# Optimization experiments

Measured on AMD Instinct MI355X. Metric: run time of the kernel, lower is better.

The kernel has to match this reference:

```python
import jax, jax.numpy as jnp
import numpy as np

B, L, H, A = 2, 384, 256, 14  # batch, total residues (binder+target), hidden, atoms/residue


def setup_inputs() -> dict:
    key = jax.random.key(0)
    ks = jax.random.split(key, 8)
    s = 1.0 / np.sqrt(H)
    h = jax.random.normal(ks[0], (B, L, H), jnp.float32)          # encoder output
    X = jax.random.normal(ks[1], (B, L, A, 3), jnp.float32)       # coordinates
    mask = jnp.ones((B, L), jnp.int32)                             # residue validity mask
    Wx_w = jax.random.normal(ks[2], (H, H), jnp.float32) * s
    Wx_b = jnp.zeros((H,), jnp.float32)
    Ux_w = jax.random.normal(ks[3], (H, H), jnp.float32) * s
    Ux_b = jnp.zeros((H,), jnp.float32)
    Tx_w = jax.random.normal(ks[4], (A, H), jnp.float32) * s
    Tx_b = jnp.zeros((A,), jnp.float32)
    return dict(h=h, X=X, mask=mask, Wx_w=Wx_w, Wx_b=Wx_b,
                Ux_w=Ux_w, Ux_b=Ux_b, Tx_w=Tx_w, Tx_b=Tx_b)


def reference(h, X, mask, Wx_w, Wx_b, Ux_w, Ux_b, Tx_w, Tx_b):
    # One recurrent coordinate-update step of FADocker._forward.
    m = mask.astype(h.dtype)                                   # (B, L)
    hw = h @ Wx_w.T + Wx_b                                     # (B, L, H)  = W_x(h)
    hu = h @ Ux_w.T + Ux_b                                     # (B, L, H)  = U_x(h)
    mij = hw[:, :, None, :] + hu[:, None, :, :]                # (B, L, L, H)
    gate = jnp.einsum('bijh,ah->bija', jax.nn.relu(mij), Tx_w) + Tx_b  # (B, L, L, A) = T_x(mij)
    xij = (X[:, :, None] - X[:, None, :]) * gate[..., None]   # (B, L, L, A, 3)
    f = jnp.einsum('bijac,bj->biac', xij, m)                   # masked sum over j
    f = f / (1e-6 + m.sum(axis=1)[:, None, None, None])        # (B, L, A, 3)
    return X + jnp.clip(f, -20.0, 20.0)
```

## Files before the change

kernel.cpp:

```cpp
#include <hip/hip_runtime.h>
#include <hip/hip_fp16.h>

#define HDIM 256
#define LDIM 384
#define BDIM 2
#define ADIM 14

typedef __attribute__((ext_vector_type(8))) _Float16 f16x8;
typedef __attribute__((ext_vector_type(2))) _Float16 f16x2;
typedef __attribute__((ext_vector_type(4))) float f32x4;

static __device__ __forceinline__ unsigned pack_f16(float x, float y) {
    f16x2 t = {(_Float16)x, (_Float16)y};
    union { f16x2 v; unsigned u; } c; c.v = t;
    return c.u;
}

static __device__ __forceinline__ unsigned relu_add(unsigned a, unsigned b) {
    union { unsigned u; f16x2 v; } ua, ub, ur;
    ua.u = a; ub.u = b;
    const f16x2 z = {(_Float16)0.f, (_Float16)0.f};
    ur.v = __builtin_elementwise_max(ua.v + ub.v, z);
    return ur.u;
}

__global__ __launch_bounds__(256) void k_front(
    const float* __restrict__ h,
    const float* __restrict__ Wx_w, const float* __restrict__ Wx_b,
    const float* __restrict__ Ux_w, const float* __restrict__ Ux_b,
    const float* __restrict__ Tx_w,
    unsigned* __restrict__ hwP, unsigned* __restrict__ huP,
    unsigned* __restrict__ txP)
{
    const int tid = threadIdx.x;
    if (blockIdx.x == 384) {
        for (int idx = tid; idx < 16 * 128; idx += 256) {
            const int a = idx >> 7, k2 = idx & 127;
            unsigned v = 0;
            if (a < ADIM) {
                const float2 tw = *(const float2*)&Tx_w[a * HDIM + 2 * k2];
                v = pack_f16(tw.x, tw.y);
            }
            txP[idx] = v;
        }
        return;
    }
    const int w = tid >> 6, lane = tid & 63;
    const int n = lane & 15, quad = lane >> 4;
    const int g = blockIdx.x * 4 + w;
    const int ctile = g & 31;
    const int rtile = g >> 5;

    const int arow = (ctile & 15) * 16 + n;
    const float* __restrict__ Arow = (ctile < 16) ? &Wx_w[arow * HDIM]
                                                  : &Ux_w[arow * HDIM];
    const float* __restrict__ Brow = &h[(rtile * 16 + n) * HDIM];

    f32x4 acc = {0.f, 0.f, 0.f, 0.f};
    #pragma unroll
    for (int kc = 0; kc < 8; ++kc) {
        const int ko = kc * 32 + quad * 8;
        const float4 a0 = *(const float4*)&Arow[ko];
        const float4 a1 = *(const float4*)&Arow[ko + 4];
        const float4 b0 = *(const float4*)&Brow[ko];
        const float4 b1 = *(const float4*)&Brow[ko + 4];
        union { unsigned u[4]; f16x8 v; } af, bf;
        af.u[0] = pack_f16(a0.x, a0.y); af.u[1] = pack_f16(a0.z, a0.w);
        af.u[2] = pack_f16(a1.x, a1.y); af.u[3] = pack_f16(a1.z, a1.w);
        bf.u[0] = pack_f16(b0.x, b0.y); bf.u[1] = pack_f16(b0.z, b0.w);
        bf.u[2] = pack_f16(b1.x, b1.y); bf.u[3] = pack_f16(b1.z, b1.w);
        acc = __builtin_amdgcn_mfma_f32_16x16x32_f16(af.v, bf.v, acc, 0, 0, 0);
    }

    const int row = rtile * 16 + n;
    const int c0 = (ctile & 15) * 16 + quad * 4;
    const float4 bias = (ctile < 16) ? *(const float4*)&Wx_b[c0]
                                     : *(const float4*)&Ux_b[c0];
    uint2 pv;
    pv.x = pack_f16(acc[0] + bias.x, acc[1] + bias.y);
    pv.y = pack_f16(acc[2] + bias.z, acc[3] + bias.w);
    unsigned* __restrict__ dst = (ctile < 16) ? hwP : huP;
    *(uint2*)&dst[row * 128 + (ctile & 15) * 8 + quad * 2] = pv;
}

__global__ __launch_bounds__(384) void k_main(
    const unsigned* __restrict__ hwP, const unsigned* __restrict__ huP,
    const unsigned* __restrict__ txP,
    const float* __restrict__ X, const int* __restrict__ mask,
    const float* __restrict__ Tx_b,
    float* __restrict__ out)
{
    __shared__ float Xl[LDIM * 42];
    __shared__ float m_lds[LDIM];
    __shared__ float part2[2][24 * 16 * 4];
    __shared__ float part_m[24];

    const int i0 = blockIdx.x * 2, i1 = i0 + 1;
    const int b  = blockIdx.y;
    const int tid = threadIdx.x;
    const int w = tid >> 6, lane = tid & 63;
    const int n = lane & 15, quad = lane >> 4;

    {
        const float4* __restrict__ Xg4 = (const float4*)&X[b * (LDIM * 42)];
        float4* __restrict__ Xl4 = (float4*)Xl;
        for (int idx = tid; idx < LDIM * 42 / 4; idx += 384) Xl4[idx] = Xg4[idx];
        m_lds[tid] = (float)mask[b * LDIM + tid];
    }
    __syncthreads();

    const unsigned* __restrict__ hwr0 = &hwP[(b * LDIM + i0) * 128];
    const unsigned* __restrict__ hwr1 = &hwP[(b * LDIM + i1) * 128];
    const unsigned* __restrict__ hub  = &huP[b * LDIM * 128];
    const unsigned* __restrict__ txr  = &txP[n * 128];

    f32x4 acc0[4], acc1[4];
    #pragma unroll
    for (int t = 0; t < 4; ++t) {
        acc0[t] = (f32x4){0.f, 0.f, 0.f, 0.f};
        acc1[t] = (f32x4){0.f, 0.f, 0.f, 0.f};
    }

    #pragma unroll 2
    for (int kc = 0; kc < 8; ++kc) {
        const int ko = kc * 16 + quad * 4;
        const uint4 hwa = *(const uint4*)&hwr0[ko];
        const uint4 hwb = *(const uint4*)&hwr1[ko];
        const uint4 tx4 = *(const uint4*)&txr[ko];
        union { unsigned u[4]; f16x8 v; } bfrag;
        bfrag.u[0] = tx4.x; bfrag.u[1] = tx4.y;
        bfrag.u[2] = tx4.z; bfrag.u[3] = tx4.w;
        #pragma unroll
        for (int t = 0; t < 4; ++t) {
            const int j = (w * 4 + t) * 16 + n;
            const uint4 hu4 = *(const uint4*)&hub[j * 128 + ko];
            union { unsigned u[4]; f16x8 v; } af;
            af.u[0] = relu_add(hwa.x, hu4.x);
            af.u[1] = relu_add(hwa.y, hu4.y);
            af.u[2] = relu_add(hwa.z, hu4.z);
            af.u[3] = relu_add(hwa.w, hu4.w);
            acc0[t] = __builtin_amdgcn_mfma_f32_16x16x32_f16(af.v, bfrag.v, acc0[t], 0, 0, 0);
            af.u[0] = relu_add(hwb.x, hu4.x);
            af.u[1] = relu_add(hwb.y, hu4.y);
            af.u[2] = relu_add(hwb.z, hu4.z);
            af.u[3] = relu_add(hwb.w, hu4.w);
            acc1[t] = __builtin_amdgcn_mfma_f32_16x16x32_f16(af.v, bfrag.v, acc1[t], 0, 0, 0);
        }
    }

    float pm = 0.f;
    #pragma unroll
    for (int ii = 0; ii < 2; ++ii) {
        const f32x4* acc = ii ? acc1 : acc0;
        float s1 = 0.f, s2x = 0.f, s2y = 0.f, s2z = 0.f;
        if (n < ADIM) {
            const float txb = Tx_b[n];
            #pragma unroll
            for (int t = 0; t < 4; ++t) {
                #pragma unroll
                for (int r = 0; r < 4; ++r) {
                    const int jd = (w * 4 + t) * 16 + quad * 4 + r;
                    const float m = m_lds[jd];
                    const float g = acc[t][r] + txb;
                    const float mg = m * g;
                    const float* __restrict__ Xp = &Xl[jd * 42 + n * 3];
                    s1 += mg;
                    s2x = fmaf(mg, Xp[0], s2x);
                    s2y = fmaf(mg, Xp[1], s2y);
                    s2z = fmaf(mg, Xp[2], s2z);
                    if (ii == 0) pm += m;
                }
            }
        }
        f32x4 sv = {s2x, s2y, s2z, s1};
        *(f32x4*)&part2[ii][((w * 4 + quad) * 16 + n) * 4] = sv;
    }
    if (n == 0) part_m[w * 4 + quad] = pm;
    __syncthreads();

    int ii = -1, t42 = 0;
    if (tid < 42)                    { ii = 0; t42 = tid; }
    else if (tid >= 64 && tid < 106) { ii = 1; t42 = tid - 64; }
    if (ii >= 0) {
        const int a = t42 / 3, c = t42 % 3;
        const int i = ii ? i1 : i0;
        float S2 = 0.f, S1 = 0.f, msum = 0.f;
        #pragma unroll 4
        for (int g = 0; g < 24; ++g) {
            const float* __restrict__ p = &part2[ii][(g * 16 + a) * 4];
            S2 += p[c]; S1 += p[3]; msum += part_m[g];
        }
        const float denom = 1e-6f + msum;
        const float xi = Xl[i * 42 + t42];
        float f = (xi * S1 - S2) / denom;
        f = fminf(fmaxf(f, -20.f), 20.f);
        out[((b * LDIM + i) * ADIM + a) * 3 + c] = xi + f;
    }
}

extern "C" void kernel_launch(void* const* d_in, const int* in_sizes, int n_in,
                              void* d_out, int out_size, void* d_ws, size_t ws_size,
                              hipStream_t stream) {
    (void)in_sizes; (void)n_in; (void)out_size; (void)ws_size;
    const float* h    = (const float*)d_in[0];
    const float* X    = (const float*)d_in[1];
    const int*   mask = (const int*)  d_in[2];
    const float* Wx_w = (const float*)d_in[3];
    const float* Wx_b = (const float*)d_in[4];
    const float* Ux_w = (const float*)d_in[5];
    const float* Ux_b = (const float*)d_in[6];
    const float* Tx_w = (const float*)d_in[7];
    const float* Tx_b = (const float*)d_in[8];
    float* out = (float*)d_out;

    unsigned* hwP = (unsigned*)d_ws;
    unsigned* huP = hwP + BDIM * LDIM * (HDIM / 2);
    unsigned* txP = huP + BDIM * LDIM * (HDIM / 2);

    k_front<<<385, 256, 0, stream>>>(h, Wx_w, Wx_b, Ux_w, Ux_b, Tx_w, hwP, huP, txP);
    k_main<<<dim3(LDIM / 2, BDIM), 384, 0, stream>>>(hwP, huP, txP, X, mask, Tx_b, out);
}
```

Before: 101.4 us.

## Stage hu chunks through LDS with prefetch, use FP32 SIMT front GEMM, drop X staging

The front projection changes from an MFMA fp16 GEMM to a 32x32 LDS-tiled fp32 FMA GEMM. It writes hu in a k-chunked layout, and the separate Tx_w packing block is removed. The main kernel stages each k-chunk of hu into padded LDS with register prefetch of the next chunk, loads and packs Tx_w fragments inline, and reads X directly from global instead of copying the whole X slab into LDS. This aims to cut global hu traffic and the large LDS X copy. In exchange it adds per-chunk barriers and a slower SIMT front GEMM.

```diff
diff --git a/kernel.cpp b/kernel.cpp
--- a/kernel.cpp
+++ b/kernel.cpp
@@ -5,6 +5,7 @@
 #define LDIM 384
 #define BDIM 2
 #define ADIM 14
+#define HBS 20
 
 typedef __attribute__((ext_vector_type(8))) _Float16 f16x8;
 typedef __attribute__((ext_vector_type(2))) _Float16 f16x2;
@@ -28,69 +29,66 @@
     const float* __restrict__ h,
     const float* __restrict__ Wx_w, const float* __restrict__ Wx_b,
     const float* __restrict__ Ux_w, const float* __restrict__ Ux_b,
-    const float* __restrict__ Tx_w,
-    unsigned* __restrict__ hwP, unsigned* __restrict__ huP,
-    unsigned* __restrict__ txP)
+    unsigned* __restrict__ hwP, unsigned* __restrict__ huK)
 {
-    const int tid = threadIdx.x;
-    if (blockIdx.x == 384) {
-        for (int idx = tid; idx < 16 * 128; idx += 256) {
-            const int a = idx >> 7, k2 = idx & 127;
-            unsigned v = 0;
-            if (a < ADIM) {
-                const float2 tw = *(const float2*)&Tx_w[a * HDIM + 2 * k2];
-                v = pack_f16(tw.x, tw.y);
-            }
-            txP[idx] = v;
-        }
-        return;
-    }
-    const int w = tid >> 6, lane = tid & 63;
-    const int n = lane & 15, quad = lane >> 4;
-    const int g = blockIdx.x * 4 + w;
-    const int ctile = g & 31;
-    const int rtile = g >> 5;
-
-    const int arow = (ctile & 15) * 16 + n;
-    const float* __restrict__ Arow = (ctile < 16) ? &Wx_w[arow * HDIM]
-                                                  : &Ux_w[arow * HDIM];
-    const float* __restrict__ Brow = &h[(rtile * 16 + n) * HDIM];
-
-    f32x4 acc = {0.f, 0.f, 0.f, 0.f};
-    #pragma unroll
-    for (int kc = 0; kc < 8; ++kc) {
-        const int ko = kc * 32 + quad * 8;
-        const float4 a0 = *(const float4*)&Arow[ko];
-        const float4 a1 = *(const float4*)&Arow[ko + 4];
-        const float4 b0 = *(const float4*)&Brow[ko];
-        const float4 b1 = *(const float4*)&Brow[ko + 4];
-        union { unsigned u[4]; f16x8 v; } af, bf;
-        af.u[0] = pack_f16(a0.x, a0.y); af.u[1] = pack_f16(a0.z, a0.w);
-        af.u[2] = pack_f16(a1.x, a1.y); af.u[3] = pack_f16(a1.z, a1.w);
-        bf.u[0] = pack_f16(b0.x, b0.y); bf.u[1] = pack_f16(b0.z, b0.w);
-        bf.u[2] = pack_f16(b1.x, b1.y); bf.u[3] = pack_f16(b1.z, b1.w);
-        acc = __builtin_amdgcn_mfma_f32_16x16x32_f16(af.v, bf.v, acc, 0, 0, 0);
-    }
-
-    const int row = rtile * 16 + n;
-    const int c0 = (ctile & 15) * 16 + quad * 4;
-    const float4 bias = (ctile < 16) ? *(const float4*)&Wx_b[c0]
-                                     : *(const float4*)&Ux_b[c0];
-    uint2 pv;
-    pv.x = pack_f16(acc[0] + bias.x, acc[1] + bias.y);
-    pv.y = pack_f16(acc[2] + bias.z, acc[3] + bias.w);
-    unsigned* __restrict__ dst = (ctile < 16) ? hwP : huP;
-    *(uint2*)&dst[row * 128 + (ctile & 15) * 8 + quad * 2] = pv;
+    __shared__ float hsT[32][34];
+    __shared__ float wsT[32][34];
+    const int t  = threadIdx.x;
+    const int tx = t & 15, ty = t >> 4;
+    const int row0 = blockIdx.y * 32;
+    const int col0 = blockIdx.x * 32;
+
+    const int lr = t & 31;
+    const int lk = (t >> 5) * 4;
+    const float* __restrict__ hrow = &h[(row0 + lr) * HDIM];
+    const int c_l = col0 + lr;
+    const float* __restrict__ wrow = (c_l < HDIM) ? &Wx_w[c_l * HDIM]
+                                                  : &Ux_w[(c_l - HDIM) * HDIM];
+
+    float a00 = 0.f, a01 = 0.f, a10 = 0.f, a11 = 0.f;
+
+    for (int k0 = 0; k0 < HDIM; k0 += 32) {
+        const float4 hv = *(const float4*)&hrow[k0 + lk];
+        const float4 wv = *(const float4*)&wrow[k0 + lk];
+        hsT[lk + 0][lr] = hv.x; hsT[lk + 1][lr] = hv.y;
+        hsT[lk + 2][lr] = hv.z; hsT[lk + 3][lr] = hv.w;
+        wsT[lk + 0][lr] = wv.x; wsT[lk + 1][lr] = wv.y;
+        wsT[lk + 2][lr] = wv.z; wsT[lk + 3][lr] = wv.w;
+        __syncthreads();
+        #pragma unroll
+        for (int kk = 0; kk < 32; ++kk) {
+            const float2 av = *(const float2*)&hsT[kk][ty * 2];
+            const float2 bv = *(const float2*)&wsT[kk][tx * 2];
+            a00 = fmaf(av.x, bv.x, a00); a01 = fmaf(av.x, bv.y, a01);
+            a10 = fmaf(av.y, bv.x, a10); a11 = fmaf(av.y, bv.y, a11);
+        }
+        __syncthreads();
+    }
+
+    const int row = row0 + ty * 2;
+    const int b = row / LDIM, i0 = row % LDIM;
+    const int c0 = col0 + tx * 2;
+    if (c0 < HDIM) {
+        const float b0 = Wx_b[c0], b1 = Wx_b[c0 + 1];
+        hwP[row * 128 + (c0 >> 1)]       = pack_f16(a00 + b0, a01 + b1);
+        hwP[(row + 1) * 128 + (c0 >> 1)] = pack_f16(a10 + b0, a11 + b1);
+    } else {
+        const int ch = c0 - HDIM;
+        const int kc = ch >> 5, d = (ch & 31) >> 1;
+        const float b0 = Ux_b[ch], b1 = Ux_b[ch + 1];
+        unsigned* __restrict__ dst = &huK[((b * 8 + kc) * LDIM) * 16 + d];
+        dst[i0 * 16]       = pack_f16(a00 + b0, a01 + b1);
+        dst[(i0 + 1) * 16] = pack_f16(a10 + b0, a11 + b1);
+    }
 }
 
 __global__ __launch_bounds__(384) void k_main(
-    const unsigned* __restrict__ hwP, const unsigned* __restrict__ huP,
-    const unsigned* __restrict__ txP,
+    const unsigned* __restrict__ hwP, const unsigned* __restrict__ huK,
+    const float* __restrict__ Tx_w, const float* __restrict__ Tx_b,
     const float* __restrict__ X, const int* __restrict__ mask,
-    const float* __restrict__ Tx_b,
     float* __restrict__ out)
 {
-    __shared__ float Xl[LDIM * 42];
+    __shared__ unsigned hbuf[LDIM * HBS];
     __shared__ float m_lds[LDIM];
     __shared__ float part2[2][24 * 16 * 4];
     __shared__ float part_m[24];
@@ -101,18 +99,12 @@
     const int w = tid >> 6, lane = tid & 63;
     const int n = lane & 15, quad = lane >> 4;
 
-    {
-        const float4* __restrict__ Xg4 = (const float4*)&X[b * (LDIM * 42)];
-        float4* __restrict__ Xl4 = (float4*)Xl;
-        for (int idx = tid; idx < LDIM * 42 / 4; idx += 384) Xl4[idx] = Xg4[idx];
-        m_lds[tid] = (float)mask[b * LDIM + tid];
-    }
-    __syncthreads();
+    m_lds[tid] = (float)mask[b * LDIM + tid];
 
     const unsigned* __restrict__ hwr0 = &hwP[(b * LDIM + i0) * 128];
     const unsigned* __restrict__ hwr1 = &hwP[(b * LDIM + i1) * 128];
-    const unsigned* __restrict__ hub  = &huP[b * LDIM * 128];
-    const unsigned* __restrict__ txr  = &txP[n * 128];
+    const unsigned* __restrict__ srcb = &huK[(b * 8) * LDIM * 16];
+    const int nn = (n < ADIM) ? n : 0;
 
     f32x4 acc0[4], acc1[4];
     #pragma unroll
@@ -121,19 +113,40 @@
         acc1[t] = (f32x4){0.f, 0.f, 0.f, 0.f};
     }
 
-    #pragma unroll 2
+    uint4 pf[4];
+    #pragma unroll
+    for (int it = 0; it < 4; ++it)
+        pf[it] = *(const uint4*)&srcb[it * 1536 + tid * 4];
+
     for (int kc = 0; kc < 8; ++kc) {
+        if (kc) __syncthreads();
+        #pragma unroll
+        for (int it = 0; it < 4; ++it) {
+            const int flat = it * 1536 + tid * 4;
+            const int jj = flat >> 4, dd = flat & 15;
+            *(uint4*)&hbuf[jj * HBS + dd] = pf[it];
+        }
+        __syncthreads();
+        if (kc < 7) {
+            #pragma unroll
+            for (int it = 0; it < 4; ++it)
+                pf[it] = *(const uint4*)&srcb[(kc + 1) * 6144 + it * 1536 + tid * 4];
+        }
+
+        const float4 t0 = *(const float4*)&Tx_w[nn * HDIM + kc * 32 + quad * 8];
+        const float4 t1 = *(const float4*)&Tx_w[nn * HDIM + kc * 32 + quad * 8 + 4];
+        union { unsigned u[4]; f16x8 v; } bfrag;
+        bfrag.u[0] = pack_f16(t0.x, t0.y); bfrag.u[1] = pack_f16(t0.z, t0.w);
+        bfrag.u[2] = pack_f16(t1.x, t1.y); bfrag.u[3] = pack_f16(t1.z, t1.w);
+
         const int ko = kc * 16 + quad * 4;
         const uint4 hwa = *(const uint4*)&hwr0[ko];
         const uint4 hwb = *(const uint4*)&hwr1[ko];
-        const uint4 tx4 = *(const uint4*)&txr[ko];
-        union { unsigned u[4]; f16x8 v; } bfrag;
-        bfrag.u[0] = tx4.x; bfrag.u[1] = tx4.y;
-        bfrag.u[2] = tx4.z; bfrag.u[3] = tx4.w;
+
         #pragma unroll
         for (int t = 0; t < 4; ++t) {
-            const int j = (w * 4 + t) * 16 + n;
-            const uint4 hu4 = *(const uint4*)&hub[j * 128 + ko];
+            const int jrow = (w * 4 + t) * 16 + n;
+            const uint4 hu4 = *(const uint4*)&hbuf[jrow * HBS + quad * 4];
             union { unsigned u[4]; f16x8 v; } af;
             af.u[0] = relu_add(hwa.x, hu4.x);
             af.u[1] = relu_add(hwa.y, hu4.y);
@@ -163,7 +176,7 @@
                     const float m = m_lds[jd];
                     const float g = acc[t][r] + txb;
                     const float mg = m * g;
-                    const float* __restrict__ Xp = &Xl[jd * 42 + n * 3];
+                    const float* __restrict__ Xp = &X[((b * LDIM + jd) * ADIM + n) * 3];
                     s1 += mg;
                     s2x = fmaf(mg, Xp[0], s2x);
                     s2y = fmaf(mg, Xp[1], s2y);
@@ -191,10 +204,11 @@
             S2 += p[c]; S1 += p[3]; msum += part_m[g];
         }
         const float denom = 1e-6f + msum;
-        const float xi = Xl[i * 42 + t42];
+        const int idx = ((b * LDIM + i) * ADIM + a) * 3 + c;
+        const float xi = X[idx];
         float f = (xi * S1 - S2) / denom;
         f = fminf(fmaxf(f, -20.f), 20.f);
-        out[((b * LDIM + i) * ADIM + a) * 3 + c] = xi + f;
+        out[idx] = xi + f;
     }
 }
 
@@ -214,9 +228,8 @@
     float* out = (float*)d_out;
 
     unsigned* hwP = (unsigned*)d_ws;
-    unsigned* huP = hwP + BDIM * LDIM * (HDIM / 2);
-    unsigned* txP = huP + BDIM * LDIM * (HDIM / 2);
-
-    k_front<<<385, 256, 0, stream>>>(h, Wx_w, Wx_b, Ux_w, Ux_b, Tx_w, hwP, huP, txP);
-    k_main<<<dim3(LDIM / 2, BDIM), 384, 0, stream>>>(hwP, huP, txP, X, mask, Tx_b, out);
-}
+    unsigned* huK = hwP + BDIM * LDIM * (HDIM / 2);
+
+    k_front<<<dim3(16, 24), 256, 0, stream>>>(h, Wx_w, Wx_b, Ux_w, Ux_b, hwP, huK);
+    k_main<<<dim3(LDIM / 2, BDIM), 384, 0, stream>>>(hwP, huK, Tx_w, Tx_b, X, mask, out);
+}
```

Measured after the change: 117.0 us. 1.15x slower.
